# Optimization experiments

Measured on AMD Instinct MI355X. Metric: run time of the kernel, lower is better.

The kernel has to match this reference:

```python
import jax, jax.numpy as jnp
import numpy as np
from jax import lax


def setup_inputs() -> dict:
    key = jax.random.key(0)
    ks = jax.random.split(key, 16)
    f32 = jnp.float32
    g = lambda k, shp, s=0.02: jax.random.normal(k, shp, dtype=f32) * s
    inp = {
        "x": jax.random.normal(ks[0], (4, 1, 4096), dtype=f32),
        # conv_time: Conv1d(1,128,3,pad=1)
        "conv_time_w": g(ks[1], (128, 1, 3)), "conv_time_b": jnp.zeros((128,), f32),
        "bn0_g": jnp.ones((128,), f32), "bn0_b": jnp.zeros((128,), f32),
        "bn0_m": jnp.zeros((128,), f32), "bn0_v": jnp.ones((128,), f32),
        # block1: Conv1d(128,256,3,pad=1)+BN
        "conv1_w": g(ks[2], (256, 128, 3)), "conv1_b": jnp.zeros((256,), f32),
        "bn1_g": jnp.ones((256,), f32), "bn1_b": jnp.zeros((256,), f32),
        "bn1_m": jnp.zeros((256,), f32), "bn1_v": jnp.ones((256,), f32),
        # block2: Conv1d(256,512,3,pad=1)+BN
        "conv2_w": g(ks[3], (512, 256, 3)), "conv2_b": jnp.zeros((512,), f32),
        "bn2_g": jnp.ones((512,), f32), "bn2_b": jnp.zeros((512,), f32),
        "bn2_m": jnp.zeros((512,), f32), "bn2_v": jnp.ones((512,), f32),
        # GAT 1: fc Linear(512,512), attn_fc Linear(1024,1)
        "gat1_fc_w": g(ks[4], (512, 512)), "gat1_fc_b": jnp.zeros((512,), f32),
        "gat1_attn_w": g(ks[5], (1024,)), "gat1_attn_b": jnp.zeros((), f32),
        # GAT 2: fc Linear(512,256), attn_fc Linear(512,1)
        "gat2_fc_w": g(ks[6], (256, 512)), "gat2_fc_b": jnp.zeros((256,), f32),
        "gat2_attn_w": g(ks[7], (512,)), "gat2_attn_b": jnp.zeros((), f32),
        # head: Linear(256,2)
        "fc_w": g(ks[8], (2, 256)), "fc_b": jnp.zeros((2,), f32),
    }
    return inp


def _conv1d(x, w, b):
    # x: [B,C,T], w: [O,C,3], padding=1
    y = lax.conv_general_dilated(x, w, window_strides=(1,), padding=((1, 1),),
                                 dimension_numbers=("NCH", "OIH", "NCH"))
    return y + b[None, :, None]


def _bn(x, g, b, m, v):
    # eval-mode BatchNorm1d over channel dim
    return (x - m[None, :, None]) * (g * lax.rsqrt(v + 1e-5))[None, :, None] + b[None, :, None]


def _maxpool2(x):
    return lax.reduce_window(x, -jnp.inf, lax.max, (1, 1, 2), (1, 1, 2), "VALID")


def _gat(x2d, fc_w, fc_b, aw, ab):
    # Faithful to: cat([h_i, h_j]) @ attn_w == h_i @ aw[:d] + h_j @ aw[d:]
    h = x2d @ fc_w.T + fc_b           # [N, d]
    d = h.shape[-1]
    s1 = h @ aw[:d]                   # [N] (query part, h.repeat(1,N))
    s2 = h @ aw[d:]                   # [N] (key part,   h.repeat(N,1))
    e = jax.nn.leaky_relu(s1[:, None] + s2[None, :] + ab, negative_slope=0.01)  # [N,N]
    att = jax.nn.softmax(e, axis=1)
    return att @ h                    # [N, d]


def reference(x, conv_time_w, conv_time_b, bn0_g, bn0_b, bn0_m, bn0_v,
              conv1_w, conv1_b, bn1_g, bn1_b, bn1_m, bn1_v,
              conv2_w, conv2_b, bn2_g, bn2_b, bn2_m, bn2_v,
              gat1_fc_w, gat1_fc_b, gat1_attn_w, gat1_attn_b,
              gat2_fc_w, gat2_fc_b, gat2_attn_w, gat2_attn_b,
              fc_w, fc_b):
    h = jax.nn.relu(_bn(_conv1d(x, conv_time_w, conv_time_b), bn0_g, bn0_b, bn0_m, bn0_v))
    h = _maxpool2(jax.nn.relu(_bn(_conv1d(h, conv1_w, conv1_b), bn1_g, bn1_b, bn1_m, bn1_v)))
    h = _maxpool2(jax.nn.relu(_bn(_conv1d(h, conv2_w, conv2_b), bn2_g, bn2_b, bn2_m, bn2_v)))
    h = jnp.transpose(h, (0, 2, 1))   # [B, S, 512]
    B, S, C = h.shape
    g = h.reshape(B * S, C)           # whole batch flattened into one graph (as in source)
    g = _gat(g, gat1_fc_w, gat1_fc_b, gat1_attn_w, gat1_attn_b)   # [N, 512]
    g = _gat(g, gat2_fc_w, gat2_fc_b, gat2_attn_w, gat2_attn_b)   # [N, 256]
    pooled = g.reshape(B, S, -1).mean(axis=1)                     # [B, 256]
    return pooled @ fc_w.T + fc_b     # [B, 2] (dropout is identity in eval)
```

## Files before the change

kernel.cpp:

```cpp
#include <hip/hip_runtime.h>
#include <hip/hip_bf16.h>
#include <math.h>


#define NN 4096
#define BB 4

__global__ void k_conv_time3(const float* __restrict__ x, const float* __restrict__ w,
                             const float* __restrict__ cb, const float* __restrict__ g,
                             const float* __restrict__ bbp, const float* __restrict__ m,
                             const float* __restrict__ v, float* __restrict__ out) {
  int gid = blockIdx.x * 256 + threadIdx.x;
  int t4 = gid & 1023;
  int o = (gid >> 10) & 127;
  int b = gid >> 17;
  int t = t4 * 4;
  float sc = g[o] * rsqrtf(v[o] + 1e-5f);
  float sh = (cb[o] - m[o]) * sc + bbp[o];
  const float* xb = x + b * 4096;
  float4 xc = *(const float4*)&xb[t];
  float xm = (t > 0) ? xb[t - 1] : 0.f;
  float xp = (t + 4 < 4096) ? xb[t + 4] : 0.f;
  const float* wo = w + o * 3;
  float w0 = wo[0], w1 = wo[1], w2 = wo[2];
  float4 y;
  y.x = fmaxf((w0 * xm   + w1 * xc.x + w2 * xc.y) * sc + sh, 0.f);
  y.y = fmaxf((w0 * xc.x + w1 * xc.y + w2 * xc.z) * sc + sh, 0.f);
  y.z = fmaxf((w0 * xc.y + w1 * xc.z + w2 * xc.w) * sc + sh, 0.f);
  y.w = fmaxf((w0 * xc.z + w1 * xc.w + w2 * xp  ) * sc + sh, 0.f);
  float* orow = out + ((size_t)(b * 128) + o) * 4104 + 4;
  *(float4*)&orow[t] = y;
  if (t4 == 0)    { orow[-4] = 0.f; orow[-3] = 0.f; orow[-2] = 0.f; orow[-1] = 0.f; }
  if (t4 == 1023) { orow[4096] = 0.f; orow[4097] = 0.f; orow[4098] = 0.f; orow[4099] = 0.f; }
}

template <int C, int TIN, int OPAD>
__global__ __launch_bounds__(64, 2)
void k_conv_fused(const float* __restrict__ in, const float* __restrict__ w,
                  const float* __restrict__ cb, const float* __restrict__ g,
                  const float* __restrict__ bbp, const float* __restrict__ m,
                  const float* __restrict__ v, float* __restrict__ out, int OCH) {
  constexpr int TOUT = TIN / 2;
  constexpr int IST = TIN + 8;
  const int OST = TOUT + 2 * OPAD;
  int nT = TIN / 256;
  int bx = blockIdx.x;
  int tb = bx % nT;
  int oq = (bx / nT) % (OCH / 8);
  int b  = bx / (nT * (OCH / 8));
  int lane = threadIdx.x;
  int t0 = tb * 256;

  float acc[8][4];
  #pragma unroll
  for (int oi = 0; oi < 8; oi++)
    #pragma unroll
    for (int p = 0; p < 4; p++) acc[oi][p] = 0.f;

  const float* wq = w + (size_t)(oq * 8) * C * 3;
  const float* xb = in + (size_t)(b * C) * IST + 4 + t0 + 4 * lane;

  float4 A = *(const float4*)(xb - 1);
  float2 Bv = *(const float2*)(xb + 3);
  for (int cc = 0; cc < C; ++cc) {
    float4 An; float2 Bn;
    if (cc + 1 < C) {
      const float* nx = xb + (size_t)(cc + 1) * IST;
      An = *(const float4*)(nx - 1);
      Bn = *(const float2*)(nx + 3);
    }
    const float* wr = wq + (size_t)cc * 3;
    #pragma unroll
    for (int oi = 0; oi < 8; oi++) {
      const float* wo = wr + (size_t)oi * C * 3;
      float w0 = wo[0], w1 = wo[1], w2 = wo[2];
      acc[oi][0] += w0 * A.x + w1 * A.y + w2 * A.z;
      acc[oi][1] += w0 * A.y + w1 * A.z + w2 * A.w;
      acc[oi][2] += w0 * A.z + w1 * A.w + w2 * Bv.x;
      acc[oi][3] += w0 * A.w + w1 * Bv.x + w2 * Bv.y;
    }
    A = An; Bv = Bn;
  }

  int base_o = oq * 8;
  #pragma unroll
  for (int oi = 0; oi < 8; oi++) {
    int o = base_o + oi;
    float sc = g[o] * rsqrtf(v[o] + 1e-5f);
    float sh = (cb[o] - m[o]) * sc + bbp[o];
    float2 r;
    r.x = fmaxf(fmaxf(acc[oi][0] * sc + sh, acc[oi][1] * sc + sh), 0.f);
    r.y = fmaxf(fmaxf(acc[oi][2] * sc + sh, acc[oi][3] * sc + sh), 0.f);
    *(float2*)&out[((size_t)(b * OCH) + o) * OST + OPAD + tb * 128 + 2 * lane] = r;
  }
  if (OPAD > 0 && tb == 0) {
    if (lane < 8) {
      float* row = out + ((size_t)(b * OCH) + base_o + lane) * OST;
      row[0] = 0.f; row[1] = 0.f; row[2] = 0.f; row[3] = 0.f;
    } else if (lane < 16) {
      float* row = out + ((size_t)(b * OCH) + base_o + lane - 8) * OST;
      row[OPAD + TOUT + 0] = 0.f; row[OPAD + TOUT + 1] = 0.f;
      row[OPAD + TOUT + 2] = 0.f; row[OPAD + TOUT + 3] = 0.f;
    }
  }
}

__global__ __launch_bounds__(512, 4)
void k_gemm_chw(const float* __restrict__ A, const float* __restrict__ Wt,
                const float* __restrict__ bias, float* __restrict__ Cout) {
  constexpr int K = 512, N = 512;
  __shared__ float As[32][132];
  __shared__ float Bs[32][68];
  int i0 = blockIdx.x * 128, j0 = blockIdx.y * 64;
  int tid = threadIdx.x;
  int tx = tid & 15, ty = tid >> 4;
  int b = i0 >> 10, s0 = i0 & 1023;
  const float* Ab = A + (size_t)b * K * 1024 + s0;

  float acc[4][4];
  #pragma unroll
  for (int ii = 0; ii < 4; ii++)
    #pragma unroll
    for (int jj = 0; jj < 4; jj++) acc[ii][jj] = 0.f;

  int ka = (tid + 0) >> 5, i4a = tid & 31;
  int kb = (tid + 512) >> 5, i4b = tid & 31;
  float4 pa0, pa1; float pb[4];

  pa0 = *(const float4*)&Ab[(size_t)ka * 1024 + 4 * i4a];
  pa1 = *(const float4*)&Ab[(size_t)kb * 1024 + 4 * i4b];
  #pragma unroll
  for (int r = 0; r < 4; r++) {
    int e = tid + 512 * r; int j = e >> 5, k = e & 31;
    pb[r] = Wt[(size_t)(j0 + j) * K + k];
  }

  for (int kt = 0; kt < K; kt += 32) {
    *(float4*)&As[ka][4 * i4a] = pa0;
    *(float4*)&As[kb][4 * i4b] = pa1;
    #pragma unroll
    for (int r = 0; r < 4; r++) {
      int e = tid + 512 * r; int j = e >> 5, k = e & 31;
      Bs[k][j] = pb[r];
    }
    __syncthreads();
    int ktn = (kt + 32 < K) ? kt + 32 : 0;
    float4 na0 = *(const float4*)&Ab[(size_t)(ktn + ka) * 1024 + 4 * i4a];
    float4 na1 = *(const float4*)&Ab[(size_t)(ktn + kb) * 1024 + 4 * i4b];
    float nb[4];
    #pragma unroll
    for (int r = 0; r < 4; r++) {
      int e = tid + 512 * r; int j = e >> 5, k = e & 31;
      nb[r] = Wt[(size_t)(j0 + j) * K + ktn + k];
    }
    #pragma unroll 4
    for (int kk = 0; kk < 32; ++kk) {
      float4 a4 = *(const float4*)&As[kk][ty * 4];
      float4 b4 = *(const float4*)&Bs[kk][tx * 4];
      float a[4] = {a4.x, a4.y, a4.z, a4.w};
      float bv[4] = {b4.x, b4.y, b4.z, b4.w};
      #pragma unroll
      for (int ii = 0; ii < 4; ii++)
        #pragma unroll
        for (int jj = 0; jj < 4; jj++) acc[ii][jj] += a[ii] * bv[jj];
    }
    __syncthreads();
    pa0 = na0; pa1 = na1;
    #pragma unroll
    for (int r = 0; r < 4; r++) pb[r] = nb[r];
  }

  float4 bias4 = *(const float4*)&bias[j0 + 4 * tx];
  #pragma unroll
  for (int ii = 0; ii < 4; ii++) {
    int i = i0 + ty * 4 + ii;
    float4 o4;
    o4.x = acc[ii][0] + bias4.x; o4.y = acc[ii][1] + bias4.y;
    o4.z = acc[ii][2] + bias4.z; o4.w = acc[ii][3] + bias4.w;
    *(float4*)&Cout[(size_t)i * N + j0 + 4 * tx] = o4;
  }
}

__global__ __launch_bounds__(256, 4)
void k_gemm_rm(const float* __restrict__ A, const float* __restrict__ Wt,
               const float* __restrict__ bias, float* __restrict__ Cout) {
  constexpr int K = 512, N = 256;
  __shared__ float As[32][68];
  __shared__ float Bs[32][68];
  int i0 = blockIdx.x * 64, j0 = blockIdx.y * 64;
  int tid = threadIdx.x;
  int tx = tid & 15, ty = tid >> 4;

  float acc[4][4];
  #pragma unroll
  for (int ii = 0; ii < 4; ii++)
    #pragma unroll
    for (int jj = 0; jj < 4; jj++) acc[ii][jj] = 0.f;

  float4 pa[2]; float pb[8];
  #pragma unroll
  for (int r = 0; r < 2; r++) {
    int e4 = tid + 256 * r; int i = e4 >> 3, k4 = e4 & 7;
    pa[r] = *(const float4*)&A[(size_t)(i0 + i) * K + 4 * k4];
  }
  #pragma unroll
  for (int r = 0; r < 8; r++) {
    int e = tid + 256 * r; int j = e >> 5, k = e & 31;
    pb[r] = Wt[(size_t)(j0 + j) * K + k];
  }

  for (int kt = 0; kt < K; kt += 32) {
    #pragma unroll
    for (int r = 0; r < 2; r++) {
      int e4 = tid + 256 * r; int i = e4 >> 3, k4 = e4 & 7;
      As[4 * k4 + 0][i] = pa[r].x; As[4 * k4 + 1][i] = pa[r].y;
      As[4 * k4 + 2][i] = pa[r].z; As[4 * k4 + 3][i] = pa[r].w;
    }
    #pragma unroll
    for (int r = 0; r < 8; r++) {
      int e = tid + 256 * r; int j = e >> 5, k = e & 31;
      Bs[k][j] = pb[r];
    }
    __syncthreads();
    int ktn = (kt + 32 < K) ? kt + 32 : 0;
    float4 na[2]; float nb[8];
    #pragma unroll
    for (int r = 0; r < 2; r++) {
      int e4 = tid + 256 * r; int i = e4 >> 3, k4 = e4 & 7;
      na[r] = *(const float4*)&A[(size_t)(i0 + i) * K + ktn + 4 * k4];
    }
    #pragma unroll
    for (int r = 0; r < 8; r++) {
      int e = tid + 256 * r; int j = e >> 5, k = e & 31;
      nb[r] = Wt[(size_t)(j0 + j) * K + ktn + k];
    }
    #pragma unroll 4
    for (int kk = 0; kk < 32; ++kk) {
      float4 a4 = *(const float4*)&As[kk][ty * 4];
      float4 b4 = *(const float4*)&Bs[kk][tx * 4];
      float a[4] = {a4.x, a4.y, a4.z, a4.w};
      float bv[4] = {b4.x, b4.y, b4.z, b4.w};
      #pragma unroll
      for (int ii = 0; ii < 4; ii++)
        #pragma unroll
        for (int jj = 0; jj < 4; jj++) acc[ii][jj] += a[ii] * bv[jj];
    }
    __syncthreads();
    pa[0] = na[0]; pa[1] = na[1];
    #pragma unroll
    for (int r = 0; r < 8; r++) pb[r] = nb[r];
  }

  float4 bias4 = *(const float4*)&bias[j0 + 4 * tx];
  #pragma unroll
  for (int ii = 0; ii < 4; ii++) {
    int i = i0 + ty * 4 + ii;
    float4 o4;
    o4.x = acc[ii][0] + bias4.x; o4.y = acc[ii][1] + bias4.y;
    o4.z = acc[ii][2] + bias4.z; o4.w = acc[ii][3] + bias4.w;
    *(float4*)&Cout[(size_t)i * N + j0 + 4 * tx] = o4;
  }
}

template <int D>
__global__ void k_rowdot(const float* __restrict__ h, const float* __restrict__ aw,
                         float* __restrict__ s1, float* __restrict__ s2,
                         int* __restrict__ rnk) {
  if (blockIdx.x < 16) rnk[blockIdx.x * 256 + threadIdx.x] = 0;
  int wid = threadIdx.x >> 6, lane = threadIdx.x & 63;
  int i = blockIdx.x * 4 + wid;
  const float* hr = h + (size_t)i * D;
  float d1 = 0.f, d2 = 0.f;
  #pragma unroll
  for (int d = lane; d < D; d += 64) {
    float hv = hr[d];
    d1 += hv * aw[d];
    d2 += hv * aw[D + d];
  }
  for (int off = 32; off; off >>= 1) {
    d1 += __shfl_down(d1, off, 64);
    d2 += __shfl_down(d2, off, 64);
  }
  if (lane == 0) { s1[i] = d1; s2[i] = d2; }
}

__global__ void k_rank(const float* __restrict__ s2v, int* __restrict__ rnk) {
  __shared__ float ls[1024];
  int j = blockIdx.x * 256 + threadIdx.x;
  int base = blockIdx.y * 1024;
  float vj = s2v[j];
  for (int e = threadIdx.x; e < 1024; e += 256) ls[e] = s2v[base + e];
  __syncthreads();
  int cnt = 0;
  #pragma unroll 8
  for (int r = 0; r < 1024; ++r) {
    float vr = ls[r];
    cnt += (vr < vj || (vr == vj && (base + r) < j)) ? 1 : 0;
  }
  atomicAdd(&rnk[j], cnt);
}

__global__ void k_scatter(const float* __restrict__ s2v, const int* __restrict__ rnk,
                          float* __restrict__ svals, int* __restrict__ sidx) {
  int j = blockIdx.x * 256 + threadIdx.x;
  int r = rnk[j];
  svals[r] = s2v[j];
  sidx[r] = j;
}

__global__ void k_tw(const float* __restrict__ s1, const float* __restrict__ svals,
                     const float* __restrict__ abp, int* __restrict__ tarr,
                     float* __restrict__ Aarr, float* __restrict__ Barr,
                     float* __restrict__ wp, float* __restrict__ wm) {
  int i = blockIdx.x * 256 + threadIdx.x;
  float ab = abp[0], M2 = svals[NN - 1];
  float alpha = s1[i] + ab;
  float cthr = -alpha;
  int lo = 0, hi = NN;
  while (lo < hi) {
    int mid = (lo + hi) >> 1;
    if (svals[mid] < cthr) lo = mid + 1; else hi = mid;
  }
  tarr[i] = lo;
  float e1 = alpha + M2;
  float gam = fmaxf(e1, 0.01f * e1);
  Aarr[i] = expf(e1 - gam);
  Barr[i] = expf(0.01f * e1 - gam);
  float d = svals[i] - M2;
  wp[i] = expf(d);
  wm[i] = expf(0.01f * d);
}

__global__ void k_scan_den(const float* __restrict__ wp, const float* __restrict__ wm,
                           float* __restrict__ preden, float* __restrict__ sufden) {
  __shared__ float csP[256], csM[256];
  int tid = threadIdx.x;
  int base = tid * 16;
  float sm = 0.f, sp = 0.f;
  for (int u = 0; u < 16; u++) { sm += wm[base + u]; sp += wp[base + u]; }
  csM[tid] = sm; csP[tid] = sp;
  __syncthreads();
  float offM = 0.f;
  for (int c = 0; c < tid; c++) offM += csM[c];
  float offP = 0.f;
  for (int c = tid + 1; c < 256; c++) offP += csP[c];
  float run = offM;
  for (int u = 0; u < 16; u++) { preden[base + u] = run; run += wm[base + u]; }
  if (tid == 255) preden[NN] = run;
  float runp = offP;
  if (tid == 255) sufden[NN] = 0.f;
  for (int u = 15; u >= 0; u--) { runp += wp[base + u]; sufden[base + u] = runp; }
}

template <int D>
__global__ void k_chunksum(const float* __restrict__ h, const int* __restrict__ sidx,
                           const float* __restrict__ wp, const float* __restrict__ wm,
                           float* __restrict__ csP, float* __restrict__ csM) {
  constexpr int CPT = D / 256;
  int c = blockIdx.x, tid = threadIdx.x;
  __shared__ int lidx[32];
  __shared__ float lwp[32], lwm[32];
  if (tid < 32) {
    int r = c * 32 + tid;
    lidx[tid] = sidx[r]; lwp[tid] = wp[r]; lwm[tid] = wm[r];
  }
  __syncthreads();
  float aP[CPT], aM[CPT];
  #pragma unroll
  for (int q = 0; q < CPT; q++) { aP[q] = 0.f; aM[q] = 0.f; }
  for (int u = 0; u < 32; u++) {
    const float* hr = h + (size_t)lidx[u] * D;
    float fp = lwp[u], fm = lwm[u];
    #pragma unroll
    for (int q = 0; q < CPT; q++) {
      float hv = hr[tid + q * 256];
      aP[q] += fp * hv; aM[q] += fm * hv;
    }
  }
  #pragma unroll
  for (int q = 0; q < CPT; q++) {
    csP[(size_t)c * D + tid + q * 256] = aP[q];
    csM[(size_t)c * D + tid + q * 256] = aM[q];
  }
}

template <int D>
__global__ void k_chunkoff(const float* __restrict__ csP, const float* __restrict__ csM,
                           float* __restrict__ offP, float* __restrict__ offM) {
  int d = blockIdx.x * 256 + threadIdx.x;
  float rm = 0.f;
  for (int cb = 0; cb < 128; cb += 16) {
    float vals[16];
    #pragma unroll
    for (int u = 0; u < 16; u++) vals[u] = csM[(size_t)(cb + u) * D + d];
    #pragma unroll
    for (int u = 0; u < 16; u++) { offM[(size_t)(cb + u) * D + d] = rm; rm += vals[u]; }
  }
  float rp = 0.f;
  for (int cb = 127; cb >= 15; cb -= 16) {
    float vals[16];
    #pragma unroll
    for (int u = 0; u < 16; u++) vals[u] = csP[(size_t)(cb - u) * D + d];
    #pragma unroll
    for (int u = 0; u < 16; u++) { offP[(size_t)(cb - u) * D + d] = rp; rp += vals[u]; }
  }
}

template <int D>
__global__ void k_scanwrite(const float* __restrict__ h, const int* __restrict__ sidx,
                            const float* __restrict__ wp, const float* __restrict__ wm,
                            const float* __restrict__ offP, const float* __restrict__ offM,
                            float* __restrict__ Pre, float* __restrict__ Suf) {
  constexpr int CPT = D / 256;
  int c = blockIdx.x, tid = threadIdx.x;
  __shared__ int lidx[32];
  __shared__ float lwp[32], lwm[32];
  if (tid < 32) {
    int r = c * 32 + tid;
    lidx[tid] = sidx[r]; lwp[tid] = wp[r]; lwm[tid] = wm[r];
  }
  __syncthreads();
  float runM[CPT], runP[CPT];
  #pragma unroll
  for (int q = 0; q < CPT; q++) {
    int d = tid + q * 256;
    runM[q] = offM[(size_t)c * D + d];
    runP[q] = offP[(size_t)c * D + d];
  }
  for (int u = 0; u < 32; u++) {
    const float* hr = h + (size_t)lidx[u] * D;
    float fm = lwm[u];
    #pragma unroll
    for (int q = 0; q < CPT; q++) {
      int d = tid + q * 256;
      Pre[(size_t)(c * 32 + u) * D + d] = runM[q];
      runM[q] += fm * hr[d];
    }
  }
  if (c == 127) {
    #pragma unroll
    for (int q = 0; q < CPT; q++) Pre[(size_t)NN * D + tid + q * 256] = runM[q];
    #pragma unroll
    for (int q = 0; q < CPT; q++) Suf[(size_t)NN * D + tid + q * 256] = 0.f;
  }
  for (int u = 31; u >= 0; u--) {
    const float* hr = h + (size_t)lidx[u] * D;
    float fp = lwp[u];
    #pragma unroll
    for (int q = 0; q < CPT; q++) {
      int d = tid + q * 256;
      runP[q] += fp * hr[d];
      Suf[(size_t)(c * 32 + u) * D + d] = runP[q];
    }
  }
}

template <int D>
__global__ void k_apply(const float* __restrict__ Pre, const float* __restrict__ Suf,
                        const float* __restrict__ preden, const float* __restrict__ sufden,
                        const int* __restrict__ tarr, const float* __restrict__ Aarr,
                        const float* __restrict__ Barr, float* __restrict__ outg) {
  int i = blockIdx.x;
  int t = tarr[i];
  float A = Aarr[i], Bv = Barr[i];
  float den = A * sufden[t] + Bv * preden[t];
  float inv = 1.f / den;
  const float* Pr = Pre + (size_t)t * D;
  const float* Sr = Suf + (size_t)t * D;
  for (int d = threadIdx.x; d < D; d += 256)
    outg[(size_t)i * D + d] = (A * Sr[d] + Bv * Pr[d]) * inv;
}

__global__ void k_pool(const float* __restrict__ g2, float* __restrict__ pp) {
  int b = blockIdx.x >> 4, ch = blockIdx.x & 15;
  const float* base = g2 + ((size_t)(b * 1024) + ch * 64) * 256 + threadIdx.x;
  float s = 0.f;
  for (int r = 0; r < 64; r++) s += base[(size_t)r * 256];
  pp[(size_t)blockIdx.x * 256 + threadIdx.x] = s;
}

__global__ void k_head2(const float* __restrict__ pp, const float* __restrict__ fcw,
                        const float* __restrict__ fcb, float* __restrict__ out) {
  __shared__ float pooled[4][256];
  int tid = threadIdx.x;
  for (int b = 0; b < 4; b++) {
    float s = 0.f;
    for (int ch = 0; ch < 16; ch++) s += pp[(size_t)(b * 16 + ch) * 256 + tid];
    pooled[b][tid] = s * (1.f / 1024.f);
  }
  __syncthreads();
  if (tid < 8) {
    int b = tid >> 1, c = tid & 1;
    float acc = fcb[c];
    for (int cc = 0; cc < 256; cc++) acc += pooled[b][cc] * fcw[c * 256 + cc];
    out[b * 2 + c] = acc;
  }
}

extern "C" void kernel_launch(void* const* d_in, const int* in_sizes, int n_in,
                              void* d_out, int out_size, void* d_ws, size_t ws_size,
                              hipStream_t stream) {
  const float* x    = (const float*)d_in[0];
  const float* ctw  = (const float*)d_in[1];
  const float* ctb  = (const float*)d_in[2];
  const float* bn0g = (const float*)d_in[3];
  const float* bn0b = (const float*)d_in[4];
  const float* bn0m = (const float*)d_in[5];
  const float* bn0v = (const float*)d_in[6];
  const float* c1w  = (const float*)d_in[7];
  const float* c1b  = (const float*)d_in[8];
  const float* bn1g = (const float*)d_in[9];
  const float* bn1b = (const float*)d_in[10];
  const float* bn1m = (const float*)d_in[11];
  const float* bn1v = (const float*)d_in[12];
  const float* c2w  = (const float*)d_in[13];
  const float* c2b  = (const float*)d_in[14];
  const float* bn2g = (const float*)d_in[15];
  const float* bn2b = (const float*)d_in[16];
  const float* bn2m = (const float*)d_in[17];
  const float* bn2v = (const float*)d_in[18];
  const float* g1w  = (const float*)d_in[19];
  const float* g1b  = (const float*)d_in[20];
  const float* g1aw = (const float*)d_in[21];
  const float* g1ab = (const float*)d_in[22];
  const float* g2w  = (const float*)d_in[23];
  const float* g2b  = (const float*)d_in[24];
  const float* g2aw = (const float*)d_in[25];
  const float* g2ab = (const float*)d_in[26];
  const float* fcw  = (const float*)d_in[27];
  const float* fcb  = (const float*)d_in[28];
  float* ws = (float*)d_ws;

  const size_t S0SZ = (size_t)4 * 128 * 4104;
  const size_t S1SZ = (size_t)4 * 256 * 2056;
  const size_t SLOT = (size_t)(NN + 1) * 512;
  float* slot0 = ws;
  float* slot1 = ws + S0SZ;
  float* slot2 = slot1 + S1SZ;
  float* slot3 = slot2 + SLOT;
  float* sm    = slot3 + SLOT;
  float* s1    = sm;
  float* s2    = sm + 4096;
  float* svals = sm + 8192;
  int*   sidx  = (int*)(sm + 12288);
  int*   tarr  = (int*)(sm + 16384);
  float* Aarr  = sm + 20480;
  float* Barr  = sm + 24576;
  float* wp    = sm + 28672;
  float* wm    = sm + 32768;
  float* preden = sm + 36864;
  float* sufden = sm + 40968;
  float* csP   = sm + 45072;
  float* csM   = csP + 65536;
  float* offP  = csM + 65536;
  float* offM  = offP + 65536;
  int*   rnk   = (int*)(offM + 65536);
  float* pp    = offM + 65536 + 4096;

  k_conv_time3<<<BB * 128 * 1024 / 256, 256, 0, stream>>>(x, ctw, ctb, bn0g, bn0b, bn0m, bn0v, slot0);
  k_conv_fused<128, 4096, 4><<<BB * 32 * 16, 64, 0, stream>>>(
      slot0, c1w, c1b, bn1g, bn1b, bn1m, bn1v, slot1, 256);
  k_conv_fused<256, 2048, 0><<<BB * 64 * 8, 64, 0, stream>>>(
      slot1, c2w, c2b, bn2g, bn2b, bn2m, bn2v, slot2, 512);

  k_gemm_chw<<<dim3(32, 8), 512, 0, stream>>>(slot2, g1w, g1b, slot3);
  k_rowdot<512><<<NN / 4, 256, 0, stream>>>(slot3, g1aw, s1, s2, rnk);
  k_rank<<<dim3(16, 4), 256, 0, stream>>>(s2, rnk);
  k_scatter<<<16, 256, 0, stream>>>(s2, rnk, svals, sidx);
  k_tw<<<NN / 256, 256, 0, stream>>>(s1, svals, g1ab, tarr, Aarr, Barr, wp, wm);
  k_scan_den<<<1, 256, 0, stream>>>(wp, wm, preden, sufden);
  k_chunksum<512><<<128, 256, 0, stream>>>(slot3, sidx, wp, wm, csP, csM);
  k_chunkoff<512><<<2, 256, 0, stream>>>(csP, csM, offP, offM);
  k_scanwrite<512><<<128, 256, 0, stream>>>(slot3, sidx, wp, wm, offP, offM, slot1, slot0);
  k_apply<512><<<NN, 256, 0, stream>>>(slot1, slot0, preden, sufden, tarr, Aarr, Barr, slot2);

  k_gemm_rm<<<dim3(64, 4), 256, 0, stream>>>(slot2, g2w, g2b, slot3);
  k_rowdot<256><<<NN / 4, 256, 0, stream>>>(slot3, g2aw, s1, s2, rnk);
  k_rank<<<dim3(16, 4), 256, 0, stream>>>(s2, rnk);
  k_scatter<<<16, 256, 0, stream>>>(s2, rnk, svals, sidx);
  k_tw<<<NN / 256, 256, 0, stream>>>(s1, svals, g2ab, tarr, Aarr, Barr, wp, wm);
  k_scan_den<<<1, 256, 0, stream>>>(wp, wm, preden, sufden);
  k_chunksum<256><<<128, 256, 0, stream>>>(slot3, sidx, wp, wm, csP, csM);
  k_chunkoff<256><<<1, 256, 0, stream>>>(csP, csM, offP, offM);
  k_scanwrite<256><<<128, 256, 0, stream>>>(slot3, sidx, wp, wm, offP, offM, slot1, slot0);
  k_apply<256><<<NN, 256, 0, stream>>>(slot1, slot0, preden, sufden, tarr, Aarr, Barr, slot2);

  k_pool<<<BB * 16, 256, 0, stream>>>(slot2, pp);
  k_head2<<<1, 256, 0, stream>>>(pp, fcw, fcb, (float*)d_out);
}
```

Measured before the change: 397.4 us.

## Halve conv output-channel tile per block and fuse rank+scatter into one kernel

The fused conv kernels now compute 4 output channels per 64-thread block instead of 8. This doubles the grid and raises the launch-bounds occupancy target, aiming to fill more CUs at the cost of re-reading inputs twice as often. The rank counting and scatter steps are merged into a single kernel that loops over all 4096 keys per thread. This removes the atomic rank buffer, its zeroing in k_rowdot, and one launch per GAT layer, but uses only 16 blocks instead of 64.

New measurement: 532.5 us. 34.0% more time.

```diff
diff --git a/kernel.cpp b/kernel.cpp
--- a/kernel.cpp
+++ b/kernel.cpp
@@ -35,29 +35,29 @@
 }
 
 template <int C, int TIN, int OPAD>
-__global__ __launch_bounds__(64, 2)
-void k_conv_fused(const float* __restrict__ in, const float* __restrict__ w,
-                  const float* __restrict__ cb, const float* __restrict__ g,
-                  const float* __restrict__ bbp, const float* __restrict__ m,
-                  const float* __restrict__ v, float* __restrict__ out, int OCH) {
+__global__ __launch_bounds__(64, 4)
+void k_conv_fused3(const float* __restrict__ in, const float* __restrict__ w,
+                   const float* __restrict__ cb, const float* __restrict__ g,
+                   const float* __restrict__ bbp, const float* __restrict__ m,
+                   const float* __restrict__ v, float* __restrict__ out, int OCH) {
   constexpr int TOUT = TIN / 2;
   constexpr int IST = TIN + 8;
   const int OST = TOUT + 2 * OPAD;
   int nT = TIN / 256;
   int bx = blockIdx.x;
   int tb = bx % nT;
-  int oq = (bx / nT) % (OCH / 8);
-  int b  = bx / (nT * (OCH / 8));
+  int oq = (bx / nT) % (OCH / 4);
+  int b  = bx / (nT * (OCH / 4));
   int lane = threadIdx.x;
   int t0 = tb * 256;
 
-  float acc[8][4];
-  #pragma unroll
-  for (int oi = 0; oi < 8; oi++)
+  float acc[4][4];
+  #pragma unroll
+  for (int oi = 0; oi < 4; oi++)
     #pragma unroll
     for (int p = 0; p < 4; p++) acc[oi][p] = 0.f;
 
-  const float* wq = w + (size_t)(oq * 8) * C * 3;
+  const float* wq = w + (size_t)(oq * 4) * C * 3;
   const float* xb = in + (size_t)(b * C) * IST + 4 + t0 + 4 * lane;
 
   float4 A = *(const float4*)(xb - 1);
@@ -71,7 +71,7 @@
     }
     const float* wr = wq + (size_t)cc * 3;
     #pragma unroll
-    for (int oi = 0; oi < 8; oi++) {
+    for (int oi = 0; oi < 4; oi++) {
       const float* wo = wr + (size_t)oi * C * 3;
       float w0 = wo[0], w1 = wo[1], w2 = wo[2];
       acc[oi][0] += w0 * A.x + w1 * A.y + w2 * A.z;
@@ -82,9 +82,9 @@
     A = An; Bv = Bn;
   }
 
-  int base_o = oq * 8;
-  #pragma unroll
-  for (int oi = 0; oi < 8; oi++) {
+  int base_o = oq * 4;
+  #pragma unroll
+  for (int oi = 0; oi < 4; oi++) {
     int o = base_o + oi;
     float sc = g[o] * rsqrtf(v[o] + 1e-5f);
     float sh = (cb[o] - m[o]) * sc + bbp[o];
@@ -94,11 +94,11 @@
     *(float2*)&out[((size_t)(b * OCH) + o) * OST + OPAD + tb * 128 + 2 * lane] = r;
   }
   if (OPAD > 0 && tb == 0) {
-    if (lane < 8) {
+    if (lane < 4) {
       float* row = out + ((size_t)(b * OCH) + base_o + lane) * OST;
       row[0] = 0.f; row[1] = 0.f; row[2] = 0.f; row[3] = 0.f;
-    } else if (lane < 16) {
-      float* row = out + ((size_t)(b * OCH) + base_o + lane - 8) * OST;
+    } else if (lane < 8) {
+      float* row = out + ((size_t)(b * OCH) + base_o + lane - 4) * OST;
       row[OPAD + TOUT + 0] = 0.f; row[OPAD + TOUT + 1] = 0.f;
       row[OPAD + TOUT + 2] = 0.f; row[OPAD + TOUT + 3] = 0.f;
     }
@@ -264,9 +264,7 @@
 
 template <int D>
 __global__ void k_rowdot(const float* __restrict__ h, const float* __restrict__ aw,
-                         float* __restrict__ s1, float* __restrict__ s2,
-                         int* __restrict__ rnk) {
-  if (blockIdx.x < 16) rnk[blockIdx.x * 256 + threadIdx.x] = 0;
+                         float* __restrict__ s1, float* __restrict__ s2) {
   int wid = threadIdx.x >> 6, lane = threadIdx.x & 63;
   int i = blockIdx.x * 4 + wid;
   const float* hr = h + (size_t)i * D;
@@ -284,28 +282,24 @@
   if (lane == 0) { s1[i] = d1; s2[i] = d2; }
 }
 
-__global__ void k_rank(const float* __restrict__ s2v, int* __restrict__ rnk) {
+__global__ void k_ranksort(const float* __restrict__ s2v, float* __restrict__ svals,
+                           int* __restrict__ sidx) {
   __shared__ float ls[1024];
   int j = blockIdx.x * 256 + threadIdx.x;
-  int base = blockIdx.y * 1024;
   float vj = s2v[j];
-  for (int e = threadIdx.x; e < 1024; e += 256) ls[e] = s2v[base + e];
-  __syncthreads();
   int cnt = 0;
-  #pragma unroll 8
-  for (int r = 0; r < 1024; ++r) {
-    float vr = ls[r];
-    cnt += (vr < vj || (vr == vj && (base + r) < j)) ? 1 : 0;
-  }
-  atomicAdd(&rnk[j], cnt);
-}
-
-__global__ void k_scatter(const float* __restrict__ s2v, const int* __restrict__ rnk,
-                          float* __restrict__ svals, int* __restrict__ sidx) {
-  int j = blockIdx.x * 256 + threadIdx.x;
-  int r = rnk[j];
-  svals[r] = s2v[j];
-  sidx[r] = j;
+  for (int base = 0; base < NN; base += 1024) {
+    __syncthreads();
+    for (int e = threadIdx.x; e < 1024; e += 256) ls[e] = s2v[base + e];
+    __syncthreads();
+    #pragma unroll 8
+    for (int r = 0; r < 1024; ++r) {
+      float vr = ls[r];
+      cnt += (vr < vj || (vr == vj && (base + r) < j)) ? 1 : 0;
+    }
+  }
+  svals[cnt] = vj;
+  sidx[cnt] = j;
 }
 
 __global__ void k_tw(const float* __restrict__ s1, const float* __restrict__ svals,
@@ -554,19 +548,17 @@
   float* csM   = csP + 65536;
   float* offP  = csM + 65536;
   float* offM  = offP + 65536;
-  int*   rnk   = (int*)(offM + 65536);
-  float* pp    = offM + 65536 + 4096;
+  float* pp    = offM + 65536;
 
   k_conv_time3<<<BB * 128 * 1024 / 256, 256, 0, stream>>>(x, ctw, ctb, bn0g, bn0b, bn0m, bn0v, slot0);
-  k_conv_fused<128, 4096, 4><<<BB * 32 * 16, 64, 0, stream>>>(
+  k_conv_fused3<128, 4096, 4><<<BB * 64 * 16, 64, 0, stream>>>(
       slot0, c1w, c1b, bn1g, bn1b, bn1m, bn1v, slot1, 256);
-  k_conv_fused<256, 2048, 0><<<BB * 64 * 8, 64, 0, stream>>>(
+  k_conv_fused3<256, 2048, 0><<<BB * 128 * 8, 64, 0, stream>>>(
       slot1, c2w, c2b, bn2g, bn2b, bn2m, bn2v, slot2, 512);
 
   k_gemm_chw<<<dim3(32, 8), 512, 0, stream>>>(slot2, g1w, g1b, slot3);
-  k_rowdot<512><<<NN / 4, 256, 0, stream>>>(slot3, g1aw, s1, s2, rnk);
-  k_rank<<<dim3(16, 4), 256, 0, stream>>>(s2, rnk);
-  k_scatter<<<16, 256, 0, stream>>>(s2, rnk, svals, sidx);
+  k_rowdot<512><<<NN / 4, 256, 0, stream>>>(slot3, g1aw, s1, s2);
+  k_ranksort<<<16, 256, 0, stream>>>(s2, svals, sidx);
   k_tw<<<NN / 256, 256, 0, stream>>>(s1, svals, g1ab, tarr, Aarr, Barr, wp, wm);
   k_scan_den<<<1, 256, 0, stream>>>(wp, wm, preden, sufden);
   k_chunksum<512><<<128, 256, 0, stream>>>(slot3, sidx, wp, wm, csP, csM);
@@ -575,9 +567,8 @@
   k_apply<512><<<NN, 256, 0, stream>>>(slot1, slot0, preden, sufden, tarr, Aarr, Barr, slot2);
 
   k_gemm_rm<<<dim3(64, 4), 256, 0, stream>>>(slot2, g2w, g2b, slot3);
-  k_rowdot<256><<<NN / 4, 256, 0, stream>>>(slot3, g2aw, s1, s2, rnk);
-  k_rank<<<dim3(16, 4), 256, 0, stream>>>(s2, rnk);
-  k_scatter<<<16, 256, 0, stream>>>(s2, rnk, svals, sidx);
+  k_rowdot<256><<<NN / 4, 256, 0, stream>>>(slot3, g2aw, s1, s2);
+  k_ranksort<<<16, 256, 0, stream>>>(s2, svals, sidx);
   k_tw<<<NN / 256, 256, 0, stream>>>(s1, svals, g2ab, tarr, Aarr, Barr, wp, wm);
   k_scan_den<<<1, 256, 0, stream>>>(wp, wm, preden, sufden);
   k_chunksum<256><<<128, 256, 0, stream>>>(slot3, sidx, wp, wm, csP, csM);
```

## Split conv input channels across two waves with shared-memory reduction

Applied to the files above, without the earlier changes.

Convolution blocks now compute 4 output channels instead of 8. Each block has two waves that each accumulate over half of the input channels, and their partial sums are combined in shared memory before BN/ReLU/maxpool. This raises the number of waves in flight to hide latency on the serial channel loop. The cost is more input reloading per output channel, plus a block barrier and an LDS reduction.

Result: faster. 367.0 us (-7.6%).

```diff
diff --git a/kernel.cpp b/kernel.cpp
--- a/kernel.cpp
+++ b/kernel.cpp
@@ -35,43 +35,48 @@
 }
 
 template <int C, int TIN, int OPAD>
-__global__ __launch_bounds__(64, 2)
-void k_conv_fused(const float* __restrict__ in, const float* __restrict__ w,
-                  const float* __restrict__ cb, const float* __restrict__ g,
-                  const float* __restrict__ bbp, const float* __restrict__ m,
-                  const float* __restrict__ v, float* __restrict__ out, int OCH) {
+__global__ __launch_bounds__(128, 8)
+void k_conv_pair(const float* __restrict__ in, const float* __restrict__ w,
+                 const float* __restrict__ cb, const float* __restrict__ g,
+                 const float* __restrict__ bbp, const float* __restrict__ m,
+                 const float* __restrict__ v, float* __restrict__ out, int OCH) {
   constexpr int TOUT = TIN / 2;
   constexpr int IST = TIN + 8;
+  constexpr int HC = C / 2;
   const int OST = TOUT + 2 * OPAD;
+  __shared__ float red[16 * 64];
+
   int nT = TIN / 256;
   int bx = blockIdx.x;
   int tb = bx % nT;
-  int oq = (bx / nT) % (OCH / 8);
-  int b  = bx / (nT * (OCH / 8));
-  int lane = threadIdx.x;
+  int oq = (bx / nT) % (OCH / 4);
+  int b  = bx / (nT * (OCH / 4));
+  int tid = threadIdx.x;
+  int lane = tid & 63;
+  int wv = __builtin_amdgcn_readfirstlane(tid >> 6);
   int t0 = tb * 256;
 
-  float acc[8][4];
-  #pragma unroll
-  for (int oi = 0; oi < 8; oi++)
+  float acc[4][4];
+  #pragma unroll
+  for (int oi = 0; oi < 4; oi++)
     #pragma unroll
     for (int p = 0; p < 4; p++) acc[oi][p] = 0.f;
 
-  const float* wq = w + (size_t)(oq * 8) * C * 3;
-  const float* xb = in + (size_t)(b * C) * IST + 4 + t0 + 4 * lane;
+  const float* wq = w + (size_t)(oq * 4) * C * 3 + (size_t)(wv * HC) * 3;
+  const float* xb = in + ((size_t)(b * C) + wv * HC) * IST + 4 + t0 + 4 * lane;
 
   float4 A = *(const float4*)(xb - 1);
   float2 Bv = *(const float2*)(xb + 3);
-  for (int cc = 0; cc < C; ++cc) {
+  for (int cc = 0; cc < HC; ++cc) {
     float4 An; float2 Bn;
-    if (cc + 1 < C) {
+    if (cc + 1 < HC) {
       const float* nx = xb + (size_t)(cc + 1) * IST;
       An = *(const float4*)(nx - 1);
       Bn = *(const float2*)(nx + 3);
     }
     const float* wr = wq + (size_t)cc * 3;
     #pragma unroll
-    for (int oi = 0; oi < 8; oi++) {
+    for (int oi = 0; oi < 4; oi++) {
       const float* wo = wr + (size_t)oi * C * 3;
       float w0 = wo[0], w1 = wo[1], w2 = wo[2];
       acc[oi][0] += w0 * A.x + w1 * A.y + w2 * A.z;
@@ -82,25 +87,39 @@
     A = An; Bv = Bn;
   }
 
-  int base_o = oq * 8;
-  #pragma unroll
-  for (int oi = 0; oi < 8; oi++) {
-    int o = base_o + oi;
-    float sc = g[o] * rsqrtf(v[o] + 1e-5f);
-    float sh = (cb[o] - m[o]) * sc + bbp[o];
-    float2 r;
-    r.x = fmaxf(fmaxf(acc[oi][0] * sc + sh, acc[oi][1] * sc + sh), 0.f);
-    r.y = fmaxf(fmaxf(acc[oi][2] * sc + sh, acc[oi][3] * sc + sh), 0.f);
-    *(float2*)&out[((size_t)(b * OCH) + o) * OST + OPAD + tb * 128 + 2 * lane] = r;
-  }
-  if (OPAD > 0 && tb == 0) {
-    if (lane < 8) {
-      float* row = out + ((size_t)(b * OCH) + base_o + lane) * OST;
-      row[0] = 0.f; row[1] = 0.f; row[2] = 0.f; row[3] = 0.f;
-    } else if (lane < 16) {
-      float* row = out + ((size_t)(b * OCH) + base_o + lane - 8) * OST;
-      row[OPAD + TOUT + 0] = 0.f; row[OPAD + TOUT + 1] = 0.f;
-      row[OPAD + TOUT + 2] = 0.f; row[OPAD + TOUT + 3] = 0.f;
+  if (wv == 1) {
+    #pragma unroll
+    for (int oi = 0; oi < 4; oi++)
+      #pragma unroll
+      for (int p = 0; p < 4; p++)
+        red[(oi * 4 + p) * 64 + lane] = acc[oi][p];
+  }
+  __syncthreads();
+  if (wv == 0) {
+    int base_o = oq * 4;
+    #pragma unroll
+    for (int oi = 0; oi < 4; oi++) {
+      int o = base_o + oi;
+      float sc = g[o] * rsqrtf(v[o] + 1e-5f);
+      float sh = (cb[o] - m[o]) * sc + bbp[o];
+      float y0 = acc[oi][0] + red[(oi * 4 + 0) * 64 + lane];
+      float y1 = acc[oi][1] + red[(oi * 4 + 1) * 64 + lane];
+      float y2 = acc[oi][2] + red[(oi * 4 + 2) * 64 + lane];
+      float y3 = acc[oi][3] + red[(oi * 4 + 3) * 64 + lane];
+      float2 r;
+      r.x = fmaxf(fmaxf(y0 * sc + sh, y1 * sc + sh), 0.f);
+      r.y = fmaxf(fmaxf(y2 * sc + sh, y3 * sc + sh), 0.f);
+      *(float2*)&out[((size_t)(b * OCH) + o) * OST + OPAD + tb * 128 + 2 * lane] = r;
+    }
+    if (OPAD > 0 && tb == 0) {
+      if (lane < 4) {
+        float* row = out + ((size_t)(b * OCH) + base_o + lane) * OST;
+        row[0] = 0.f; row[1] = 0.f; row[2] = 0.f; row[3] = 0.f;
+      } else if (lane < 8) {
+        float* row = out + ((size_t)(b * OCH) + base_o + lane - 4) * OST;
+        row[OPAD + TOUT + 0] = 0.f; row[OPAD + TOUT + 1] = 0.f;
+        row[OPAD + TOUT + 2] = 0.f; row[OPAD + TOUT + 3] = 0.f;
+      }
     }
   }
 }
@@ -558,9 +577,9 @@
   float* pp    = offM + 65536 + 4096;
 
   k_conv_time3<<<BB * 128 * 1024 / 256, 256, 0, stream>>>(x, ctw, ctb, bn0g, bn0b, bn0m, bn0v, slot0);
-  k_conv_fused<128, 4096, 4><<<BB * 32 * 16, 64, 0, stream>>>(
+  k_conv_pair<128, 4096, 4><<<BB * 64 * 16, 128, 0, stream>>>(
       slot0, c1w, c1b, bn1g, bn1b, bn1m, bn1v, slot1, 256);
-  k_conv_fused<256, 2048, 0><<<BB * 64 * 8, 64, 0, stream>>>(
+  k_conv_pair<256, 2048, 0><<<BB * 128 * 8, 128, 0, stream>>>(
       slot1, c2w, c2b, bn2g, bn2b, bn2m, bn2v, slot2, 512);
 
   k_gemm_chw<<<dim3(32, 8), 512, 0, stream>>>(slot2, g1w, g1b, slot3);
```
